# Kernel optimization log

Hardware: AMD Instinct MI355X
Metric: run time of the kernel (lower is better)

## Reference

```python
import jax, jax.numpy as jnp
import numpy as np

WINDOW_SIZE = 5  # hardcoded in module __init__


def local_window_mask(T, dtype=jnp.float32):
    # Faithful to torch code: start from triu(ones, diagonal=1) (value 1.0 for
    # j > i, NOT -inf!), then set entries outside the band |j - i| <= sz to -inf.
    sz = WINDOW_SIZE // 2
    i = jnp.arange(T)[:, None]
    j = jnp.arange(T)[None, :]
    upper = (j > i).astype(dtype)            # triu part contributes +1 bias
    in_band = jnp.abs(j - i) <= sz
    return jnp.where(in_band, upper, jnp.float32(-jnp.inf).astype(dtype))


def setup_inputs() -> dict:
    key = jax.random.key(0)
    kx, kq, kk, kv = jax.random.split(key, 4)
    B, T, C = 4, 4096, 64
    head_size = 64
    s = 1.0 / np.sqrt(C)
    return {
        "x": jax.random.normal(kx, (B, T, C), dtype=jnp.float32),
        "Wq": jax.random.normal(kq, (head_size, C), dtype=jnp.float32) * s,
        "Wk": jax.random.normal(kk, (head_size, C), dtype=jnp.float32) * s,
        "Wv": jax.random.normal(kv, (head_size, C), dtype=jnp.float32) * s,
    }


def reference(x, Wq, Wk, Wv):
    B, T, C = x.shape
    # nn.Linear(d_model, head_size, bias=False): y = x @ W.T
    q = jnp.einsum('btc,hc->bth', x, Wq)
    k = jnp.einsum('btc,hc->bth', x, Wk)
    v = jnp.einsum('btc,hc->bth', x, Wv)
    scale = jnp.asarray(C, x.dtype) ** -0.5   # scale uses input dim C
    scores = jnp.einsum('bth,bsh->bts', q, k) * scale + local_window_mask(T, x.dtype)
    attn = jax.nn.softmax(scores, axis=-1)    # original computes this twice; once suffices (same math)
    op = jnp.einsum('bts,bsh->bth', attn, v)
    return (op, attn)
```

## Files before the change

kernel.cpp:

```cpp
#include <hip/hip_runtime.h>

constexpr int B      = 4;
constexpr int T      = 4096;
constexpr int C      = 64;
constexpr int H      = 64;
constexpr int TILE   = 32;
constexpr int HALO   = 2;
constexpr int HR     = TILE + 2 * HALO;
constexpr int LS     = 68;
constexpr int NT     = 256;
constexpr int NTILES = T / TILE;

__device__ __forceinline__ void compute_mat(float (*__restrict__ dst)[LS],
                                            const float (*__restrict__ sXl)[LS],
                                            const float (*__restrict__ sWl)[LS],
                                            const int rows, const int srcOff,
                                            const int tid)
{
    const int nrt = rows >> 2;
    if (tid < nrt * 8) {
        const int rt = tid >> 3;
        const int h0 = (tid & 7) << 3;
        int r[4];
#pragma unroll
        for (int k = 0; k < 4; ++k) r[k] = rt + k * nrt + srcOff;

        float acc[4][8];
#pragma unroll
        for (int k = 0; k < 4; ++k)
#pragma unroll
            for (int j = 0; j < 8; ++j) acc[k][j] = 0.f;

        for (int c4 = 0; c4 < C; c4 += 4) {
            float xv[4][4];
#pragma unroll
            for (int k = 0; k < 4; ++k)
                *(float4*)&xv[k][0] = *(const float4*)&sXl[r[k]][c4];
#pragma unroll
            for (int cc = 0; cc < 4; ++cc) {
                const float4 wA = *(const float4*)&sWl[c4 + cc][h0];
                const float4 wB = *(const float4*)&sWl[c4 + cc][h0 + 4];
#pragma unroll
                for (int k = 0; k < 4; ++k) {
                    const float xs = xv[k][cc];
                    acc[k][0] = fmaf(xs, wA.x, acc[k][0]);
                    acc[k][1] = fmaf(xs, wA.y, acc[k][1]);
                    acc[k][2] = fmaf(xs, wA.z, acc[k][2]);
                    acc[k][3] = fmaf(xs, wA.w, acc[k][3]);
                    acc[k][4] = fmaf(xs, wB.x, acc[k][4]);
                    acc[k][5] = fmaf(xs, wB.y, acc[k][5]);
                    acc[k][6] = fmaf(xs, wB.z, acc[k][6]);
                    acc[k][7] = fmaf(xs, wB.w, acc[k][7]);
                }
            }
        }
#pragma unroll
        for (int k = 0; k < 4; ++k) {
            const int rr = r[k] - srcOff;
            *(float4*)&dst[rr][h0]     = make_float4(acc[k][0], acc[k][1], acc[k][2], acc[k][3]);
            *(float4*)&dst[rr][h0 + 4] = make_float4(acc[k][4], acc[k][5], acc[k][6], acc[k][7]);
        }
    }
}

__global__ __launch_bounds__(NT, 2)
void sparse_attn_fused(const float* __restrict__ x,
                       const float* __restrict__ Wq,
                       const float* __restrict__ Wk,
                       const float* __restrict__ Wv,
                       float* __restrict__ out)
{
    __shared__ float sX[HR][LS];
    __shared__ float sW[C][LS];
    __shared__ float sQ[TILE][LS];
    __shared__ float sK[HR][LS];
    __shared__ float sV[HR][LS];
    __shared__ float sS[TILE][8];

    const int tid  = threadIdx.x;
    const int b    = blockIdx.x / NTILES;
    const int tile = blockIdx.x % NTILES;
    const int row0 = tile * TILE;
    const float* xb = x + (size_t)b * T * C;
    const size_t attnBase = (size_t)B * T * H;
    float* attnBlock = out + attnBase + ((size_t)b * T + row0) * T;

    for (int s = tid; s < HR * (C / 4); s += NT) {
        const int lr = s >> 4;
        const int c4 = (s & 15) << 2;
        const int gr = row0 + lr - HALO;
        float4 v = make_float4(0.f, 0.f, 0.f, 0.f);
        if (gr >= 0 && gr < T) v = *(const float4*)(xb + (size_t)gr * C + c4);
        *(float4*)&sX[lr][c4] = v;
    }
    for (int s = tid; s < C * H; s += NT) sW[s & 63][s >> 6] = Wq[s];
    {
        float4* dst = (float4*)attnBlock;
        const float4 z = make_float4(0.f, 0.f, 0.f, 0.f);
        for (int s = tid; s < TILE * (T / 4); s += NT) dst[s] = z;
    }
    __syncthreads();

    compute_mat(sQ, sX, sW, TILE, HALO, tid);
    __syncthreads();

    for (int s = tid; s < C * H; s += NT) sW[s & 63][s >> 6] = Wk[s];
    __syncthreads();

    compute_mat(sK, sX, sW, HR, 0, tid);
    __syncthreads();

    if (tid < TILE * 5) {
        const int i  = tid / 5;
        const int dj = tid % 5;
        const int jg = row0 + i - HALO + dj;
        float sc = -__builtin_inff();
        if (jg >= 0 && jg < T) {
            float acc = 0.f;
#pragma unroll
            for (int h4 = 0; h4 < C; h4 += 4) {
                const float4 q = *(const float4*)&sQ[i][h4];
                const float4 k = *(const float4*)&sK[i + dj][h4];
                acc += q.x * k.x + q.y * k.y + q.z * k.z + q.w * k.w;
            }
            sc = acc * 0.125f + (dj > 2 ? 1.0f : 0.0f);
        }
        sS[i][dj] = sc;
    }
    for (int s = tid; s < C * H; s += NT) sW[s & 63][s >> 6] = Wv[s];
    __syncthreads();

    if (tid < TILE) {
        const int i  = tid;
        const int ig = row0 + i;
        float sc[5];
        float m = -__builtin_inff();
#pragma unroll
        for (int d = 0; d < 5; ++d) { sc[d] = sS[i][d]; m = fmaxf(m, sc[d]); }
        float p[5];
        float sum = 0.f;
#pragma unroll
        for (int d = 0; d < 5; ++d) { p[d] = expf(sc[d] - m); sum += p[d]; }
        const float inv = 1.f / sum;
        float* rowp = out + attnBase + ((size_t)b * T + ig) * T;
#pragma unroll
        for (int d = 0; d < 5; ++d) {
            const float pv = p[d] * inv;
            sS[i][d] = pv;
            const int j = ig - HALO + d;
            if (j >= 0 && j < T) rowp[j] = pv;
        }
    }
    __syncthreads();

    compute_mat(sV, sX, sW, HR, 0, tid);
    __syncthreads();

    for (int s = tid; s < TILE * H; s += NT) {
        const int h = s & 63;
        const int r = s >> 6;
        float acc = 0.f;
#pragma unroll
        for (int d = 0; d < 5; ++d) acc = fmaf(sS[r][d], sV[r + d][h], acc);
        out[((size_t)b * T + row0 + r) * H + h] = acc;
    }
}

extern "C" void kernel_launch(void* const* d_in, const int* in_sizes, int n_in,
                              void* d_out, int out_size, void* d_ws, size_t ws_size,
                              hipStream_t stream) {
    (void)in_sizes; (void)n_in; (void)d_ws; (void)ws_size; (void)out_size;
    const float* x  = (const float*)d_in[0];
    const float* Wq = (const float*)d_in[1];
    const float* Wk = (const float*)d_in[2];
    const float* Wv = (const float*)d_in[3];
    float* out = (float*)d_out;
    sparse_attn_fused<<<dim3(B * NTILES), dim3(NT), 0, stream>>>(x, Wq, Wk, Wv, out);
}
```

Before: 283.2 us.

## Write attention rows in one pass and compute QKV with register-held weights

The attention matrix is no longer zero-filled first and then overwritten with scattered scalar stores. Each row's band values are staged into an 8-float buffer aligned to a float4 boundary, and a single float4 pass writes zeros plus the band values. The shared weight tile and the tiled matmul helper are removed. Each thread now holds one weight row in registers and computes Q, K and V dot products directly, which removes three weight transposes through shared memory and several barriers. The PV output also uses float4 stores. The cost is higher register pressure from the 16 float4 weight registers, which may reduce occupancy.

Result: slower. 449.0 us (+58.5%).

```diff
diff --git a/kernel.cpp b/kernel.cpp
--- a/kernel.cpp
+++ b/kernel.cpp
@@ -11,58 +11,6 @@
 constexpr int NT     = 256;
 constexpr int NTILES = T / TILE;
 
-__device__ __forceinline__ void compute_mat(float (*__restrict__ dst)[LS],
-                                            const float (*__restrict__ sXl)[LS],
-                                            const float (*__restrict__ sWl)[LS],
-                                            const int rows, const int srcOff,
-                                            const int tid)
-{
-    const int nrt = rows >> 2;
-    if (tid < nrt * 8) {
-        const int rt = tid >> 3;
-        const int h0 = (tid & 7) << 3;
-        int r[4];
-#pragma unroll
-        for (int k = 0; k < 4; ++k) r[k] = rt + k * nrt + srcOff;
-
-        float acc[4][8];
-#pragma unroll
-        for (int k = 0; k < 4; ++k)
-#pragma unroll
-            for (int j = 0; j < 8; ++j) acc[k][j] = 0.f;
-
-        for (int c4 = 0; c4 < C; c4 += 4) {
-            float xv[4][4];
-#pragma unroll
-            for (int k = 0; k < 4; ++k)
-                *(float4*)&xv[k][0] = *(const float4*)&sXl[r[k]][c4];
-#pragma unroll
-            for (int cc = 0; cc < 4; ++cc) {
-                const float4 wA = *(const float4*)&sWl[c4 + cc][h0];
-                const float4 wB = *(const float4*)&sWl[c4 + cc][h0 + 4];
-#pragma unroll
-                for (int k = 0; k < 4; ++k) {
-                    const float xs = xv[k][cc];
-                    acc[k][0] = fmaf(xs, wA.x, acc[k][0]);
-                    acc[k][1] = fmaf(xs, wA.y, acc[k][1]);
-                    acc[k][2] = fmaf(xs, wA.z, acc[k][2]);
-                    acc[k][3] = fmaf(xs, wA.w, acc[k][3]);
-                    acc[k][4] = fmaf(xs, wB.x, acc[k][4]);
-                    acc[k][5] = fmaf(xs, wB.y, acc[k][5]);
-                    acc[k][6] = fmaf(xs, wB.z, acc[k][6]);
-                    acc[k][7] = fmaf(xs, wB.w, acc[k][7]);
-                }
-            }
-        }
-#pragma unroll
-        for (int k = 0; k < 4; ++k) {
-            const int rr = r[k] - srcOff;
-            *(float4*)&dst[rr][h0]     = make_float4(acc[k][0], acc[k][1], acc[k][2], acc[k][3]);
-            *(float4*)&dst[rr][h0 + 4] = make_float4(acc[k][4], acc[k][5], acc[k][6], acc[k][7]);
-        }
-    }
-}
-
 __global__ __launch_bounds__(NT, 2)
 void sparse_attn_fused(const float* __restrict__ x,
                        const float* __restrict__ Wq,
@@ -71,19 +19,18 @@
                        float* __restrict__ out)
 {
     __shared__ float sX[HR][LS];
-    __shared__ float sW[C][LS];
     __shared__ float sQ[TILE][LS];
     __shared__ float sK[HR][LS];
     __shared__ float sV[HR][LS];
     __shared__ float sS[TILE][8];
+    __shared__ float sBV[TILE][8];
+    __shared__ int   sBG[TILE];
 
     const int tid  = threadIdx.x;
     const int b    = blockIdx.x / NTILES;
     const int tile = blockIdx.x % NTILES;
     const int row0 = tile * TILE;
     const float* xb = x + (size_t)b * T * C;
-    const size_t attnBase = (size_t)B * T * H;
-    float* attnBlock = out + attnBase + ((size_t)b * T + row0) * T;
 
     for (int s = tid; s < HR * (C / 4); s += NT) {
         const int lr = s >> 4;
@@ -93,21 +40,65 @@
         if (gr >= 0 && gr < T) v = *(const float4*)(xb + (size_t)gr * C + c4);
         *(float4*)&sX[lr][c4] = v;
     }
-    for (int s = tid; s < C * H; s += NT) sW[s & 63][s >> 6] = Wq[s];
-    {
-        float4* dst = (float4*)attnBlock;
-        const float4 z = make_float4(0.f, 0.f, 0.f, 0.f);
-        for (int s = tid; s < TILE * (T / 4); s += NT) dst[s] = z;
-    }
-    __syncthreads();
-
-    compute_mat(sQ, sX, sW, TILE, HALO, tid);
-    __syncthreads();
-
-    for (int s = tid; s < C * H; s += NT) sW[s & 63][s >> 6] = Wk[s];
-    __syncthreads();
-
-    compute_mat(sK, sX, sW, HR, 0, tid);
+
+    const int h = tid & 63;
+    const int w = tid >> 6;
+
+    float4 wr[16];
+#pragma unroll
+    for (int c4 = 0; c4 < 16; ++c4) wr[c4] = *(const float4*)(Wq + h * C + c4 * 4);
+
+    __syncthreads();
+
+#pragma unroll
+    for (int ii = 0; ii < 8; ++ii) {
+        const int i = w * 8 + ii;
+        float acc = 0.f;
+#pragma unroll
+        for (int c4 = 0; c4 < 16; ++c4) {
+            const float4 xv = *(const float4*)&sX[i + HALO][c4 * 4];
+            acc = fmaf(xv.x, wr[c4].x, acc);
+            acc = fmaf(xv.y, wr[c4].y, acc);
+            acc = fmaf(xv.z, wr[c4].z, acc);
+            acc = fmaf(xv.w, wr[c4].w, acc);
+        }
+        sQ[i][h] = acc;
+    }
+
+#pragma unroll
+    for (int c4 = 0; c4 < 16; ++c4) wr[c4] = *(const float4*)(Wk + h * C + c4 * 4);
+#pragma unroll
+    for (int ii = 0; ii < 9; ++ii) {
+        const int l = w * 9 + ii;
+        float acc = 0.f;
+#pragma unroll
+        for (int c4 = 0; c4 < 16; ++c4) {
+            const float4 xv = *(const float4*)&sX[l][c4 * 4];
+            acc = fmaf(xv.x, wr[c4].x, acc);
+            acc = fmaf(xv.y, wr[c4].y, acc);
+            acc = fmaf(xv.z, wr[c4].z, acc);
+            acc = fmaf(xv.w, wr[c4].w, acc);
+        }
+        sK[l][h] = acc;
+    }
+
+#pragma unroll
+    for (int c4 = 0; c4 < 16; ++c4) wr[c4] = *(const float4*)(Wv + h * C + c4 * 4);
+#pragma unroll
+    for (int ii = 0; ii < 9; ++ii) {
+        const int l = w * 9 + ii;
+        float acc = 0.f;
+#pragma unroll
+        for (int c4 = 0; c4 < 16; ++c4) {
+            const float4 xv = *(const float4*)&sX[l][c4 * 4];
+            acc = fmaf(xv.x, wr[c4].x, acc);
+            acc = fmaf(xv.y, wr[c4].y, acc);
+            acc = fmaf(xv.z, wr[c4].z, acc);
+            acc = fmaf(xv.w, wr[c4].w, acc);
+        }
+        sV[l][h] = acc;
+    }
+
     __syncthreads();
 
     if (tid < TILE * 5) {
@@ -118,16 +109,18 @@
         if (jg >= 0 && jg < T) {
             float acc = 0.f;
 #pragma unroll
-            for (int h4 = 0; h4 < C; h4 += 4) {
-                const float4 q = *(const float4*)&sQ[i][h4];
-                const float4 k = *(const float4*)&sK[i + dj][h4];
-                acc += q.x * k.x + q.y * k.y + q.z * k.z + q.w * k.w;
+            for (int c4 = 0; c4 < C; c4 += 4) {
+                const float4 q = *(const float4*)&sQ[i][c4];
+                const float4 k = *(const float4*)&sK[i + dj][c4];
+                acc = fmaf(q.x, k.x, acc);
+                acc = fmaf(q.y, k.y, acc);
+                acc = fmaf(q.z, k.z, acc);
+                acc = fmaf(q.w, k.w, acc);
             }
             sc = acc * 0.125f + (dj > 2 ? 1.0f : 0.0f);
         }
         sS[i][dj] = sc;
     }
-    for (int s = tid; s < C * H; s += NT) sW[s & 63][s >> 6] = Wv[s];
     __syncthreads();
 
     if (tid < TILE) {
@@ -142,27 +135,59 @@
 #pragma unroll
         for (int d = 0; d < 5; ++d) { p[d] = expf(sc[d] - m); sum += p[d]; }
         const float inv = 1.f / sum;
-        float* rowp = out + attnBase + ((size_t)b * T + ig) * T;
+
+        const int j0   = ig - HALO;
+        const int G0   = (j0 > 0 ? j0 : 0) >> 2;
+        const int base = G0 << 2;
+        float bw[8];
+#pragma unroll
+        for (int q = 0; q < 8; ++q) bw[q] = 0.f;
 #pragma unroll
         for (int d = 0; d < 5; ++d) {
             const float pv = p[d] * inv;
             sS[i][d] = pv;
-            const int j = ig - HALO + d;
-            if (j >= 0 && j < T) rowp[j] = pv;
-        }
-    }
-    __syncthreads();
-
-    compute_mat(sV, sX, sW, HR, 0, tid);
-    __syncthreads();
-
-    for (int s = tid; s < TILE * H; s += NT) {
-        const int h = s & 63;
-        const int r = s >> 6;
-        float acc = 0.f;
-#pragma unroll
-        for (int d = 0; d < 5; ++d) acc = fmaf(sS[r][d], sV[r + d][h], acc);
-        out[((size_t)b * T + row0 + r) * H + h] = acc;
+            const int off = j0 + d - base;
+            if (off >= 0 && off < 8) bw[off] = pv;
+        }
+        sBG[i] = G0;
+#pragma unroll
+        for (int q = 0; q < 8; ++q) sBV[i][q] = bw[q];
+    }
+    __syncthreads();
+
+
+    for (int s = tid; s < TILE * (H / 4); s += NT) {
+        const int r  = s >> 4;
+        const int hq = (s & 15) << 2;
+        float4 acc = make_float4(0.f, 0.f, 0.f, 0.f);
+#pragma unroll
+        for (int d = 0; d < 5; ++d) {
+            const float pv = sS[r][d];
+            const float4 vv = *(const float4*)&sV[r + d][hq];
+            acc.x = fmaf(pv, vv.x, acc.x);
+            acc.y = fmaf(pv, vv.y, acc.y);
+            acc.z = fmaf(pv, vv.z, acc.z);
+            acc.w = fmaf(pv, vv.w, acc.w);
+        }
+        *(float4*)(out + ((size_t)b * T + row0 + r) * H + hq) = acc;
+    }
+
+    const size_t attnBase = (size_t)B * T * H;
+    float4* dst = (float4*)(out + attnBase + ((size_t)b * T + row0) * T);
+    const float4 z = make_float4(0.f, 0.f, 0.f, 0.f);
+    for (int rr = 0; rr < TILE; ++rr) {
+        const int   G0 = sBG[rr];
+        const float4 V0 = *(const float4*)&sBV[rr][0];
+        const float4 V1 = *(const float4*)&sBV[rr][4];
+        float4* drow = dst + rr * (T / 4);
+#pragma unroll
+        for (int kk = 0; kk < 4; ++kk) {
+            const int g = kk * NT + tid;
+            float4 v = z;
+            if (g == G0)          v = V0;
+            else if (g == G0 + 1) v = V1;
+            drow[g] = v;
+        }
     }
 }
 
```
